# Performance work log

Measured on AMD Instinct MI355X. Metric: run time of the kernel, lower is better.

## Reference

```python
import jax, jax.numpy as jnp
import numpy as np

N_NODES = 50000
N_EDGES = 800000
NODE_DIM = 8
EDGE_DIM = 4
ENC = 64
ROUNDS = 3
OUT_DIM = 5
NEG_SLOPE = 0.2


def _segment_softmax(s, dst, n):
    # per-destination-neighborhood softmax over edge scores s: [E]
    smax = jax.ops.segment_max(s, dst, num_segments=n)
    ex = jnp.exp(s - smax[dst])
    denom = jax.ops.segment_sum(ex, dst, num_segments=n)
    return ex / denom[dst]


def _gatv2(h, e_enc, src, dst, Wl, Wr, We, att, b):
    # GATv2Conv, heads=1, share_weights=False, no dropout (eval)
    xl = h @ Wl            # [N, ENC] source transform
    xr = h @ Wr            # [N, ENC] dest transform
    ep = e_enc @ We        # [E, ENC] edge transform
    m = xl[src] + xr[dst] + ep               # [E, ENC]
    s = jax.nn.leaky_relu(m, NEG_SLOPE) @ att  # [E]
    alpha = _segment_softmax(s, dst, h.shape[0])
    out = jax.ops.segment_sum(alpha[:, None] * xl[src], dst, num_segments=h.shape[0])
    return out + b


def _gnn_stack(h, e_enc, src, dst, Wl, Wr, We, att, b):
    for r in range(ROUNDS):
        h = _gatv2(h, e_enc, src, dst, Wl[r], Wr[r], We[r], att[r], b[r])
        if r < ROUNDS - 1:
            h = jax.nn.relu(h)
    return h


def setup_inputs() -> dict:
    key = jax.random.key(0)
    ks = jax.random.split(key, 24)
    f32 = jnp.float32
    p = lambda k, shp: 0.1 * jax.random.normal(k, shp, dtype=f32)
    return {
        "x": jax.random.normal(ks[0], (N_NODES, NODE_DIM), dtype=f32),
        "edge_attr": jax.random.normal(ks[1], (N_EDGES, EDGE_DIM), dtype=f32),
        "W_node": p(ks[2], (NODE_DIM, ENC)), "b_node": jnp.zeros((ENC,), f32),
        "W_edge": p(ks[3], (EDGE_DIM, ENC)), "b_edge": jnp.zeros((ENC,), f32),
        "actor_Wl": p(ks[4], (ROUNDS, ENC, ENC)),
        "actor_Wr": p(ks[5], (ROUNDS, ENC, ENC)),
        "actor_We": p(ks[6], (ROUNDS, ENC, ENC)),
        "actor_att": p(ks[7], (ROUNDS, ENC)),
        "actor_b": jnp.zeros((ROUNDS, ENC), f32),
        "critic_Wl": p(ks[8], (ROUNDS, ENC, ENC)),
        "critic_Wr": p(ks[9], (ROUNDS, ENC, ENC)),
        "critic_We": p(ks[10], (ROUNDS, ENC, ENC)),
        "critic_att": p(ks[11], (ROUNDS, ENC)),
        "critic_b": jnp.zeros((ROUNDS, ENC), f32),
        "W_act": p(ks[12], (ENC, OUT_DIM)), "b_act": jnp.zeros((OUT_DIM,), f32),
        "W_val": p(ks[13], (ENC, 1)), "b_val": jnp.zeros((1,), f32),
        "src": jax.random.randint(ks[14], (N_EDGES,), 0, N_NODES, dtype=jnp.int32),
        "dst": jax.random.randint(ks[15], (N_EDGES,), 0, N_NODES, dtype=jnp.int32),
    }


def reference(x, edge_attr, W_node, b_node, W_edge, b_edge,
              actor_Wl, actor_Wr, actor_We, actor_att, actor_b,
              critic_Wl, critic_Wr, critic_We, critic_att, critic_b,
              W_act, b_act, W_val, b_val, src, dst):
    h0 = x @ W_node + b_node          # node encoder (single SlimFC, no activation)
    e0 = edge_attr @ W_edge + b_edge  # edge encoder
    ha = _gnn_stack(h0, e0, src, dst, actor_Wl, actor_Wr, actor_We, actor_att, actor_b)
    hc = _gnn_stack(h0, e0, src, dst, critic_Wl, critic_Wr, critic_We, critic_att, critic_b)
    actions = jnp.tanh(ha @ W_act + b_act)  # action decoder, tanh activation
    values = hc @ W_val + b_val             # value decoder, no activation
    return jnp.concatenate([actions, values], axis=-1)  # [N, OUT_DIM+1]
```

## Files before the change

kernel.cpp:

```cpp
#include <hip/hip_runtime.h>
#include <math.h>

#define N_NODES 50000
#define N_EDGES 800000
#define ENC 64
#define ROUNDS 3
#define NEG_SLOPE 0.2f

typedef unsigned int u32;

__device__ __forceinline__ float lrelu(float m) {
  return m > 0.f ? m : NEG_SLOPE * m;
}

__global__ void k_hist(const int* __restrict__ dst, int* __restrict__ deg) {
  int i = blockIdx.x * blockDim.x + threadIdx.x;
  int stride = gridDim.x * blockDim.x;
  for (; i < N_EDGES; i += stride) atomicAdd(&deg[dst[i]], 1);
}

#define SCAN_BLOCKS ((N_NODES + 255) / 256)

__global__ void __launch_bounds__(256) k_red(const int* __restrict__ deg,
                                             int* __restrict__ part) {
  __shared__ int sm[256];
  int bi = blockIdx.x, t = threadIdx.x;
  int i = bi * 256 + t;
  sm[t] = (i < N_NODES) ? deg[i] : 0;
  __syncthreads();
  for (int off = 128; off > 0; off >>= 1) {
    if (t < off) sm[t] += sm[t + off];
    __syncthreads();
  }
  if (t == 0) part[bi] = sm[0];
}

__global__ void __launch_bounds__(256) k_scanp(int* __restrict__ part) {
  __shared__ int sm[256];
  int t = threadIdx.x;
  int v = (t < SCAN_BLOCKS) ? part[t] : 0;
  sm[t] = v;
  __syncthreads();
  for (int off = 1; off < 256; off <<= 1) {
    int u = (t >= off) ? sm[t - off] : 0;
    __syncthreads();
    sm[t] += u;
    __syncthreads();
  }
  if (t < SCAN_BLOCKS) part[t] = sm[t] - v;
}

__global__ void __launch_bounds__(256) k_csr(int* __restrict__ degcur,
                                             const int* __restrict__ part,
                                             int* __restrict__ row_start) {
  __shared__ int sm[256];
  int bi = blockIdx.x, t = threadIdx.x;
  int i = bi * 256 + t;
  int v = (i < N_NODES) ? degcur[i] : 0;
  sm[t] = v;
  __syncthreads();
  for (int off = 1; off < 256; off <<= 1) {
    int u = (t >= off) ? sm[t - off] : 0;
    __syncthreads();
    sm[t] += u;
    __syncthreads();
  }
  int excl = sm[t] - v + part[bi];
  if (i < N_NODES) {
    row_start[i] = excl;
    degcur[i] = excl;
    if (i == N_NODES - 1) row_start[N_NODES] = excl + v;
  }
}

__global__ void k_scatter(const int* __restrict__ src, const int* __restrict__ dst,
                          const float* __restrict__ ea, int* __restrict__ cursor,
                          int* __restrict__ srcs, float* __restrict__ ea_perm) {
  int i = blockIdx.x * blockDim.x + threadIdx.x;
  int stride = gridDim.x * blockDim.x;
  for (; i < N_EDGES; i += stride) {
    int d = dst[i];
    int pos = atomicAdd(&cursor[d], 1);
    srcs[pos] = src[i];
    ((float4*)ea_perm)[pos] = ((const float4*)ea)[i];
  }
}

__global__ void k_wcomb(const float* __restrict__ W_edge, const float* __restrict__ b_edge,
                        const float* __restrict__ aWe, const float* __restrict__ cWe,
                        float* __restrict__ wcomb, float* __restrict__ bcomb) {
  int t = threadIdx.x;
  int i = t >> 6, d = t & 63;
  for (int sr = 0; sr < 6; ++sr) {
    const float* We = (sr < 3) ? (aWe + sr * ENC * ENC) : (cWe + (sr - 3) * ENC * ENC);
    float sum = 0.f;
    for (int k = 0; k < ENC; ++k) sum += W_edge[i * ENC + k] * We[k * ENC + d];
    wcomb[sr * 4 * ENC + i * ENC + d] = sum;
    if (t < ENC) {
      float bs = 0.f;
      for (int k = 0; k < ENC; ++k) bs += b_edge[k] * We[k * ENC + t];
      bcomb[sr * ENC + t] = bs;
    }
  }
}

__global__ void k_encode(const float* __restrict__ x, const float* __restrict__ Wn,
                         const float* __restrict__ bn, float* __restrict__ h0) {
  __shared__ float lw[8 * ENC];
  __shared__ float lb[ENC];
  int t = threadIdx.x;
  for (int i = t; i < 8 * ENC; i += blockDim.x) lw[i] = Wn[i];
  if (t < ENC) lb[t] = bn[t];
  __syncthreads();
  int wid = t >> 6, lane = t & 63;
  int nwaves = (blockDim.x >> 6) * gridDim.x;
  int w = blockIdx.x * (blockDim.x >> 6) + wid;
  for (int n = w; n < N_NODES; n += nwaves) {
    const float4* xr4 = (const float4*)(x + n * 8);
    float4 a = xr4[0], b = xr4[1];
    float acc = lb[lane];
    acc += a.x * lw[0 * ENC + lane] + a.y * lw[1 * ENC + lane] +
           a.z * lw[2 * ENC + lane] + a.w * lw[3 * ENC + lane];
    acc += b.x * lw[4 * ENC + lane] + b.y * lw[5 * ENC + lane] +
           b.z * lw[6 * ENC + lane] + b.w * lw[7 * ENC + lane];
    h0[n * ENC + lane] = acc;
  }
}

__global__ void __launch_bounds__(256) k_gemm2(const float* __restrict__ hinA,
                                               const float* __restrict__ hinC,
                                               const float* __restrict__ WlA,
                                               const float* __restrict__ WrA,
                                               const float* __restrict__ bcA,
                                               float* __restrict__ xlA_,
                                               float* __restrict__ xrA_,
                                               const float* __restrict__ WlC,
                                               const float* __restrict__ WrC,
                                               const float* __restrict__ bcC,
                                               float* __restrict__ xlC_,
                                               float* __restrict__ xrC_) {
  const int stk = blockIdx.y;
  const float* hin = stk ? hinC : hinA;
  const float* Wl = stk ? WlC : WlA;
  const float* Wr = stk ? WrC : WrA;
  const float* bc = stk ? bcC : bcA;
  float* xl = stk ? xlC_ : xlA_;
  float* xr = stk ? xrC_ : xrA_;
  __shared__ float lw[2 * ENC * ENC];
  __shared__ float lh[64 * ENC];
  int t = threadIdx.x;
  {
    const float4* wl4 = (const float4*)Wl;
    const float4* wr4 = (const float4*)Wr;
    float4* lw4 = (float4*)lw;
#pragma unroll
    for (int i = 0; i < 4; ++i) lw4[t + 256 * i] = wl4[t + 256 * i];
#pragma unroll
    for (int i = 0; i < 4; ++i) lw4[1024 + t + 256 * i] = wr4[t + 256 * i];
  }
  int base = blockIdx.x * 64;
  {
    const float4* h4 = (const float4*)hin;
    float4* lh4 = (float4*)lh;
    int maxi = N_NODES * 16 - 1;
#pragma unroll
    for (int i = 0; i < 4; ++i) {
      int idx = t + 256 * i;
      int gi = base * 16 + idx;
      if (gi > maxi) gi = maxi;
      lh4[idx] = h4[gi];
    }
  }
  __syncthreads();
  int wid = t >> 6, lane = t & 63;
  int msel = lane >> 5, cc = lane & 31;
  const float2* lw2 = (const float2*)lw;
  float* outp = msel ? xr : xl;
  float2 bcv = make_float2(0.f, 0.f);
  if (msel) bcv = ((const float2*)bc)[cc];
#pragma unroll
  for (int chunk = 0; chunk < 4; ++chunk) {
    int n0 = wid * 16 + chunk * 4;
    float a00 = 0.f, a01 = 0.f, a10 = 0.f, a11 = 0.f;
    float a20 = 0.f, a21 = 0.f, a30 = 0.f, a31 = 0.f;
    const float4* r0 = (const float4*)(lh + (n0 + 0) * ENC);
    const float4* r1 = (const float4*)(lh + (n0 + 1) * ENC);
    const float4* r2 = (const float4*)(lh + (n0 + 2) * ENC);
    const float4* r3 = (const float4*)(lh + (n0 + 3) * ENC);
#pragma unroll
    for (int k4 = 0; k4 < 16; ++k4) {
      float4 h0 = r0[k4], h1 = r1[k4], h2 = r2[k4], h3 = r3[k4];
      float2 w0 = lw2[msel * 2048 + (k4 * 4 + 0) * 32 + cc];
      float2 w1 = lw2[msel * 2048 + (k4 * 4 + 1) * 32 + cc];
      float2 w2 = lw2[msel * 2048 + (k4 * 4 + 2) * 32 + cc];
      float2 w3 = lw2[msel * 2048 + (k4 * 4 + 3) * 32 + cc];
      a00 += h0.x * w0.x + h0.y * w1.x + h0.z * w2.x + h0.w * w3.x;
      a01 += h0.x * w0.y + h0.y * w1.y + h0.z * w2.y + h0.w * w3.y;
      a10 += h1.x * w0.x + h1.y * w1.x + h1.z * w2.x + h1.w * w3.x;
      a11 += h1.x * w0.y + h1.y * w1.y + h1.z * w2.y + h1.w * w3.y;
      a20 += h2.x * w0.x + h2.y * w1.x + h2.z * w2.x + h2.w * w3.x;
      a21 += h2.x * w0.y + h2.y * w1.y + h2.z * w2.y + h2.w * w3.y;
      a30 += h3.x * w0.x + h3.y * w1.x + h3.z * w2.x + h3.w * w3.x;
      a31 += h3.x * w0.y + h3.y * w1.y + h3.z * w2.y + h3.w * w3.y;
    }
    int ng = base + n0;
    if (ng + 0 < N_NODES) *(float2*)(outp + (size_t)(ng + 0) * ENC + cc * 2) = make_float2(a00 + bcv.x, a01 + bcv.y);
    if (ng + 1 < N_NODES) *(float2*)(outp + (size_t)(ng + 1) * ENC + cc * 2) = make_float2(a10 + bcv.x, a11 + bcv.y);
    if (ng + 2 < N_NODES) *(float2*)(outp + (size_t)(ng + 2) * ENC + cc * 2) = make_float2(a20 + bcv.x, a21 + bcv.y);
    if (ng + 3 < N_NODES) *(float2*)(outp + (size_t)(ng + 3) * ENC + cc * 2) = make_float2(a30 + bcv.x, a31 + bcv.y);
  }
}

template <int RELU>
__global__ void __launch_bounds__(256) k_attn(
    const int* __restrict__ row_start, const int* __restrict__ srcs,
    const float* __restrict__ ea_perm,
    const float* __restrict__ xla, const float* __restrict__ xra,
    const float* __restrict__ xlc, const float* __restrict__ xrc,
    const float* __restrict__ wca, const float* __restrict__ wcc,
    const float* __restrict__ atta, const float* __restrict__ attc,
    const float* __restrict__ Ba, const float* __restrict__ Bc,
    float* __restrict__ ha, float* __restrict__ hc) {
  const float NEG_INF = __int_as_float(0xff800000u);
  int t = threadIdx.x;
  int wid = t >> 6, lane = t & 63;
  int g = lane >> 4;
  int l16 = lane & 15;
  float4 wa0 = ((const float4*)(wca + 0 * ENC))[l16];
  float4 wa1 = ((const float4*)(wca + 1 * ENC))[l16];
  float4 wa2 = ((const float4*)(wca + 2 * ENC))[l16];
  float4 wa3 = ((const float4*)(wca + 3 * ENC))[l16];
  float4 wc0 = ((const float4*)(wcc + 0 * ENC))[l16];
  float4 wc1 = ((const float4*)(wcc + 1 * ENC))[l16];
  float4 wc2 = ((const float4*)(wcc + 2 * ENC))[l16];
  float4 wc3 = ((const float4*)(wcc + 3 * ENC))[l16];
  float4 ata = ((const float4*)atta)[l16];
  float4 atc = ((const float4*)attc)[l16];
  float4 bva = ((const float4*)Ba)[l16];
  float4 bvc = ((const float4*)Bc)[l16];
  int nw = (blockDim.x >> 6) * gridDim.x;
  for (int n = blockIdx.x * (blockDim.x >> 6) + wid; n < N_NODES; n += nw) {
    int rs = row_start[n], re = row_start[n + 1];
    float4 outa, outc;
    if (re > rs) {
      float4 xran = ((const float4*)(xra + (size_t)n * ENC))[l16];
      float4 xrcn = ((const float4*)(xrc + (size_t)n * ENC))[l16];
      float ma = -1e30f, mc = -1e30f, dena = 0.f, denc = 0.f;
      float4 acca = make_float4(0.f, 0.f, 0.f, 0.f);
      float4 accc = make_float4(0.f, 0.f, 0.f, 0.f);
      for (int base = rs; base < re; base += 16) {
        int cnt = re - base;
        if (cnt > 16) cnt = 16;
        float eav = (lane < 4 * cnt) ? ea_perm[(size_t)base * 4 + lane] : 0.f;
        int sval = (lane < cnt) ? srcs[base + lane] : 0;
#pragma unroll
        for (int j = 0; j < 4; ++j) {
          if (j * 4 >= cnt) break;
          int jj = j * 4 + g;
          bool act = jj < cnt;
          int sn = __shfl(sval, act ? jj : 0);
          float av0 = __shfl(eav, jj * 4 + 0);
          float av1 = __shfl(eav, jj * 4 + 1);
          float av2 = __shfl(eav, jj * 4 + 2);
          float av3 = __shfl(eav, jj * 4 + 3);
          int idx = sn * 16 + l16;
          float4 la = ((const float4*)xla)[idx];
          float4 lc = ((const float4*)xlc)[idx];
          float px = lrelu(la.x + xran.x + av0 * wa0.x + av1 * wa1.x + av2 * wa2.x + av3 * wa3.x) * ata.x;
          px += lrelu(la.y + xran.y + av0 * wa0.y + av1 * wa1.y + av2 * wa2.y + av3 * wa3.y) * ata.y;
          px += lrelu(la.z + xran.z + av0 * wa0.z + av1 * wa1.z + av2 * wa2.z + av3 * wa3.z) * ata.z;
          px += lrelu(la.w + xran.w + av0 * wa0.w + av1 * wa1.w + av2 * wa2.w + av3 * wa3.w) * ata.w;
          float py = lrelu(lc.x + xrcn.x + av0 * wc0.x + av1 * wc1.x + av2 * wc2.x + av3 * wc3.x) * atc.x;
          py += lrelu(lc.y + xrcn.y + av0 * wc0.y + av1 * wc1.y + av2 * wc2.y + av3 * wc3.y) * atc.y;
          py += lrelu(lc.z + xrcn.z + av0 * wc0.z + av1 * wc1.z + av2 * wc2.z + av3 * wc3.z) * atc.z;
          py += lrelu(lc.w + xrcn.w + av0 * wc0.w + av1 * wc1.w + av2 * wc2.w + av3 * wc3.w) * atc.w;
          px += __shfl_xor(px, 1); py += __shfl_xor(py, 1);
          px += __shfl_xor(px, 2); py += __shfl_xor(py, 2);
          px += __shfl_xor(px, 4); py += __shfl_xor(py, 4);
          px += __shfl_xor(px, 8); py += __shfl_xor(py, 8);
          px = act ? px : NEG_INF;
          py = act ? py : NEG_INF;
          float mna = fmaxf(ma, px);
          float sca = __expf(ma - mna);
          float exa = __expf(px - mna);
          dena = dena * sca + exa;
          acca.x = acca.x * sca + exa * la.x;
          acca.y = acca.y * sca + exa * la.y;
          acca.z = acca.z * sca + exa * la.z;
          acca.w = acca.w * sca + exa * la.w;
          ma = mna;
          float mnc = fmaxf(mc, py);
          float scc = __expf(mc - mnc);
          float exc = __expf(py - mnc);
          denc = denc * scc + exc;
          accc.x = accc.x * scc + exc * lc.x;
          accc.y = accc.y * scc + exc * lc.y;
          accc.z = accc.z * scc + exc * lc.z;
          accc.w = accc.w * scc + exc * lc.w;
          mc = mnc;
        }
      }
#pragma unroll
      for (int d = 16; d <= 32; d <<= 1) {
        float m2 = __shfl_xor(ma, d);
        float dn2 = __shfl_xor(dena, d);
        float a2x = __shfl_xor(acca.x, d), a2y = __shfl_xor(acca.y, d);
        float a2z = __shfl_xor(acca.z, d), a2w = __shfl_xor(acca.w, d);
        float mn = fmaxf(ma, m2);
        float s1 = __expf(ma - mn), s2 = __expf(m2 - mn);
        dena = dena * s1 + dn2 * s2;
        acca.x = acca.x * s1 + a2x * s2;
        acca.y = acca.y * s1 + a2y * s2;
        acca.z = acca.z * s1 + a2z * s2;
        acca.w = acca.w * s1 + a2w * s2;
        ma = mn;
        m2 = __shfl_xor(mc, d);
        dn2 = __shfl_xor(denc, d);
        a2x = __shfl_xor(accc.x, d); a2y = __shfl_xor(accc.y, d);
        a2z = __shfl_xor(accc.z, d); a2w = __shfl_xor(accc.w, d);
        mn = fmaxf(mc, m2);
        s1 = __expf(mc - mn); s2 = __expf(m2 - mn);
        denc = denc * s1 + dn2 * s2;
        accc.x = accc.x * s1 + a2x * s2;
        accc.y = accc.y * s1 + a2y * s2;
        accc.z = accc.z * s1 + a2z * s2;
        accc.w = accc.w * s1 + a2w * s2;
        mc = mn;
      }
      float ia = 1.f / dena, ic = 1.f / denc;
      outa = make_float4(acca.x * ia + bva.x, acca.y * ia + bva.y,
                         acca.z * ia + bva.z, acca.w * ia + bva.w);
      outc = make_float4(accc.x * ic + bvc.x, accc.y * ic + bvc.y,
                         accc.z * ic + bvc.z, accc.w * ic + bvc.w);
    } else {
      outa = bva;
      outc = bvc;
    }
    if (RELU) {
      outa.x = fmaxf(outa.x, 0.f); outa.y = fmaxf(outa.y, 0.f);
      outa.z = fmaxf(outa.z, 0.f); outa.w = fmaxf(outa.w, 0.f);
      outc.x = fmaxf(outc.x, 0.f); outc.y = fmaxf(outc.y, 0.f);
      outc.z = fmaxf(outc.z, 0.f); outc.w = fmaxf(outc.w, 0.f);
    }
    if (g == 0) {
      ((float4*)(ha + (size_t)n * ENC))[l16] = outa;
      ((float4*)(hc + (size_t)n * ENC))[l16] = outc;
    }
  }
}

__global__ void k_dec(const float* __restrict__ ha, const float* __restrict__ hc,
                      const float* __restrict__ Wa, const float* __restrict__ ba,
                      const float* __restrict__ Wv, const float* __restrict__ bv,
                      float* __restrict__ out) {
  int t = threadIdx.x;
  int wid = t >> 6, lane = t & 63;
  int nw = (blockDim.x >> 6) * gridDim.x;
  int w = blockIdx.x * (blockDim.x >> 6) + wid;
  for (int n = w; n < N_NODES; n += nw) {
    float hva = ha[(size_t)n * ENC + lane];
    float hvc = hc[(size_t)n * ENC + lane];
#pragma unroll
    for (int j = 0; j < 5; ++j) {
      float p = hva * Wa[lane * 5 + j];
      p += __shfl_xor(p, 1);
      p += __shfl_xor(p, 2);
      p += __shfl_xor(p, 4);
      p += __shfl_xor(p, 8);
      p += __shfl_xor(p, 16);
      p += __shfl_xor(p, 32);
      if (lane == 0) out[n * 6 + j] = tanhf(p + ba[j]);
    }
    float p = hvc * Wv[lane];
    p += __shfl_xor(p, 1);
    p += __shfl_xor(p, 2);
    p += __shfl_xor(p, 4);
    p += __shfl_xor(p, 8);
    p += __shfl_xor(p, 16);
    p += __shfl_xor(p, 32);
    if (lane == 0) out[n * 6 + 5] = p + bv[0];
  }
}

extern "C" void kernel_launch(void* const* d_in, const int* in_sizes, int n_in,
                              void* d_out, int out_size, void* d_ws, size_t ws_size,
                              hipStream_t stream) {
  const float* x    = (const float*)d_in[0];
  const float* ea   = (const float*)d_in[1];
  const float* Wn   = (const float*)d_in[2];
  const float* bn   = (const float*)d_in[3];
  const float* Wedg = (const float*)d_in[4];
  const float* bedg = (const float*)d_in[5];
  const float* aWl  = (const float*)d_in[6];
  const float* aWr  = (const float*)d_in[7];
  const float* aWe  = (const float*)d_in[8];
  const float* aAtt = (const float*)d_in[9];
  const float* aB   = (const float*)d_in[10];
  const float* cWl  = (const float*)d_in[11];
  const float* cWr  = (const float*)d_in[12];
  const float* cWe  = (const float*)d_in[13];
  const float* cAtt = (const float*)d_in[14];
  const float* cB   = (const float*)d_in[15];
  const float* Wa   = (const float*)d_in[16];
  const float* ba   = (const float*)d_in[17];
  const float* Wv   = (const float*)d_in[18];
  const float* bv   = (const float*)d_in[19];
  const int* src    = (const int*)d_in[20];
  const int* dst    = (const int*)d_in[21];
  float* out = (float*)d_out;

  char* w = (char*)d_ws;
  size_t off = 0;
  auto alloc = [&](size_t bytes) -> char* {
    char* p = w + off;
    off = (off + bytes + 255) & ~(size_t)255;
    return p;
  };
  float* h0  = (float*)alloc((size_t)N_NODES * ENC * 4);
  float* hA  = (float*)alloc((size_t)N_NODES * ENC * 4);
  float* hC  = (float*)alloc((size_t)N_NODES * ENC * 4);
  float* xlA = (float*)alloc((size_t)N_NODES * ENC * 4);
  float* xrA = (float*)alloc((size_t)N_NODES * ENC * 4);
  float* xlC = (float*)alloc((size_t)N_NODES * ENC * 4);
  float* xrC = (float*)alloc((size_t)N_NODES * ENC * 4);
  int* srcs      = (int*)alloc((size_t)N_EDGES * 4);
  float* ea_perm = (float*)alloc((size_t)N_EDGES * 16);
  int* row_start = (int*)alloc((size_t)(N_NODES + 1) * 4);
  int* cursor    = (int*)alloc((size_t)N_NODES * 4);
  int* part      = (int*)alloc(256 * 4);
  float* wcomb   = (float*)alloc(6 * 4 * ENC * 4);
  float* bcomb   = (float*)alloc(6 * ENC * 4);

  hipMemsetAsync(cursor, 0, (size_t)N_NODES * 4, stream);
  k_hist<<<2048, 256, 0, stream>>>(dst, cursor);
  k_red<<<SCAN_BLOCKS, 256, 0, stream>>>(cursor, part);
  k_scanp<<<1, 256, 0, stream>>>(part);
  k_csr<<<SCAN_BLOCKS, 256, 0, stream>>>(cursor, part, row_start);
  k_scatter<<<2048, 256, 0, stream>>>(src, dst, ea, cursor, srcs, ea_perm);

  k_wcomb<<<1, 256, 0, stream>>>(Wedg, bedg, aWe, cWe, wcomb, bcomb);
  k_encode<<<512, 256, 0, stream>>>(x, Wn, bn, h0);

  const int GEMM_TILES = (N_NODES + 63) / 64;

  for (int r = 0; r < ROUNDS; ++r) {
    const float* hinA = (r == 0) ? h0 : hA;
    const float* hinC = (r == 0) ? h0 : hC;
    k_gemm2<<<dim3(GEMM_TILES, 2), 256, 0, stream>>>(
        hinA, hinC, aWl + r * ENC * ENC, aWr + r * ENC * ENC, bcomb + r * ENC, xlA, xrA,
        cWl + r * ENC * ENC, cWr + r * ENC * ENC, bcomb + (3 + r) * ENC, xlC, xrC);
    if (r < ROUNDS - 1)
      k_attn<1><<<2048, 256, 0, stream>>>(row_start, srcs, ea_perm, xlA, xrA, xlC, xrC,
                                          wcomb + r * 4 * ENC, wcomb + (3 + r) * 4 * ENC,
                                          aAtt + r * ENC, cAtt + r * ENC,
                                          aB + r * ENC, cB + r * ENC, hA, hC);
    else
      k_attn<0><<<2048, 256, 0, stream>>>(row_start, srcs, ea_perm, xlA, xrA, xlC, xrC,
                                          wcomb + r * 4 * ENC, wcomb + (3 + r) * 4 * ENC,
                                          aAtt + r * ENC, cAtt + r * ENC,
                                          aB + r * ENC, cB + r * ENC, hA, hC);
  }
  k_dec<<<1024, 256, 0, stream>>>(hA, hC, Wa, ba, Wv, bv, out);
}
```

Baseline: 787.6 us.

## Split attention kernel by actor/critic stack and prefetch next edge chunk

The attention kernel now handles one stack per block via blockIdx.y instead of processing actor and critic together in each wave. This halves register pressure per wave and doubles the grid. Within each chunk, all four neighbour gathers are issued before any compute, and the next chunk's source indices and edge attributes are prefetched, to overlap memory latency. The weight-combination kernel is folded into block 0 of the encode kernel to save a launch. The trade-off is that CSR metadata and edge attributes are now read twice, once per stack.

```diff
diff --git a/kernel.cpp b/kernel.cpp
--- a/kernel.cpp
+++ b/kernel.cpp
@@ -86,29 +86,28 @@
   }
 }
 
-__global__ void k_wcomb(const float* __restrict__ W_edge, const float* __restrict__ b_edge,
-                        const float* __restrict__ aWe, const float* __restrict__ cWe,
-                        float* __restrict__ wcomb, float* __restrict__ bcomb) {
-  int t = threadIdx.x;
-  int i = t >> 6, d = t & 63;
-  for (int sr = 0; sr < 6; ++sr) {
-    const float* We = (sr < 3) ? (aWe + sr * ENC * ENC) : (cWe + (sr - 3) * ENC * ENC);
-    float sum = 0.f;
-    for (int k = 0; k < ENC; ++k) sum += W_edge[i * ENC + k] * We[k * ENC + d];
-    wcomb[sr * 4 * ENC + i * ENC + d] = sum;
-    if (t < ENC) {
-      float bs = 0.f;
-      for (int k = 0; k < ENC; ++k) bs += b_edge[k] * We[k * ENC + t];
-      bcomb[sr * ENC + t] = bs;
-    }
-  }
-}
-
 __global__ void k_encode(const float* __restrict__ x, const float* __restrict__ Wn,
-                         const float* __restrict__ bn, float* __restrict__ h0) {
+                         const float* __restrict__ bn, float* __restrict__ h0,
+                         const float* __restrict__ W_edge, const float* __restrict__ b_edge,
+                         const float* __restrict__ aWe, const float* __restrict__ cWe,
+                         float* __restrict__ wcomb, float* __restrict__ bcomb) {
   __shared__ float lw[8 * ENC];
   __shared__ float lb[ENC];
   int t = threadIdx.x;
+  if (blockIdx.x == 0) {
+    int i = t >> 6, d = t & 63;
+    for (int sr = 0; sr < 6; ++sr) {
+      const float* We = (sr < 3) ? (aWe + sr * ENC * ENC) : (cWe + (sr - 3) * ENC * ENC);
+      float sum = 0.f;
+      for (int k = 0; k < ENC; ++k) sum += W_edge[i * ENC + k] * We[k * ENC + d];
+      wcomb[sr * 4 * ENC + i * ENC + d] = sum;
+      if (t < ENC) {
+        float bs = 0.f;
+        for (int k = 0; k < ENC; ++k) bs += b_edge[k] * We[k * ENC + t];
+        bcomb[sr * ENC + t] = bs;
+      }
+    }
+  }
   for (int i = t; i < 8 * ENC; i += blockDim.x) lw[i] = Wn[i];
   if (t < ENC) lb[t] = bn[t];
   __syncthreads();
@@ -222,130 +221,112 @@
     const float* __restrict__ Ba, const float* __restrict__ Bc,
     float* __restrict__ ha, float* __restrict__ hc) {
   const float NEG_INF = __int_as_float(0xff800000u);
+  const int stk = blockIdx.y;
+  const float* xl = stk ? xlc : xla;
+  const float* xr = stk ? xrc : xra;
+  const float* wc = stk ? wcc : wca;
+  const float* att = stk ? attc : atta;
+  const float* B = stk ? Bc : Ba;
+  float* hout = stk ? hc : ha;
   int t = threadIdx.x;
   int wid = t >> 6, lane = t & 63;
   int g = lane >> 4;
   int l16 = lane & 15;
-  float4 wa0 = ((const float4*)(wca + 0 * ENC))[l16];
-  float4 wa1 = ((const float4*)(wca + 1 * ENC))[l16];
-  float4 wa2 = ((const float4*)(wca + 2 * ENC))[l16];
-  float4 wa3 = ((const float4*)(wca + 3 * ENC))[l16];
-  float4 wc0 = ((const float4*)(wcc + 0 * ENC))[l16];
-  float4 wc1 = ((const float4*)(wcc + 1 * ENC))[l16];
-  float4 wc2 = ((const float4*)(wcc + 2 * ENC))[l16];
-  float4 wc3 = ((const float4*)(wcc + 3 * ENC))[l16];
-  float4 ata = ((const float4*)atta)[l16];
-  float4 atc = ((const float4*)attc)[l16];
-  float4 bva = ((const float4*)Ba)[l16];
-  float4 bvc = ((const float4*)Bc)[l16];
+  float4 w0 = ((const float4*)(wc + 0 * ENC))[l16];
+  float4 w1 = ((const float4*)(wc + 1 * ENC))[l16];
+  float4 w2 = ((const float4*)(wc + 2 * ENC))[l16];
+  float4 w3 = ((const float4*)(wc + 3 * ENC))[l16];
+  float4 at = ((const float4*)att)[l16];
+  float4 bv = ((const float4*)B)[l16];
   int nw = (blockDim.x >> 6) * gridDim.x;
   for (int n = blockIdx.x * (blockDim.x >> 6) + wid; n < N_NODES; n += nw) {
     int rs = row_start[n], re = row_start[n + 1];
-    float4 outa, outc;
+    float4 outv;
     if (re > rs) {
-      float4 xran = ((const float4*)(xra + (size_t)n * ENC))[l16];
-      float4 xrcn = ((const float4*)(xrc + (size_t)n * ENC))[l16];
-      float ma = -1e30f, mc = -1e30f, dena = 0.f, denc = 0.f;
-      float4 acca = make_float4(0.f, 0.f, 0.f, 0.f);
-      float4 accc = make_float4(0.f, 0.f, 0.f, 0.f);
+      float4 xrn = ((const float4*)(xr + (size_t)n * ENC))[l16];
+      float m = -1e30f, den = 0.f;
+      float4 acc = make_float4(0.f, 0.f, 0.f, 0.f);
+      int cnt0 = re - rs; if (cnt0 > 16) cnt0 = 16;
+      float eav = (lane < 4 * cnt0) ? ea_perm[(size_t)rs * 4 + lane] : 0.f;
+      int sval = (lane < cnt0) ? srcs[rs + lane] : 0;
       for (int base = rs; base < re; base += 16) {
-        int cnt = re - base;
-        if (cnt > 16) cnt = 16;
-        float eav = (lane < 4 * cnt) ? ea_perm[(size_t)base * 4 + lane] : 0.f;
-        int sval = (lane < cnt) ? srcs[base + lane] : 0;
+        int cnt = re - base; if (cnt > 16) cnt = 16;
+        float eav_c = eav;
+        int sval_c = sval;
+        int nb = base + 16;
+        if (nb < re) {
+          int cn = re - nb; if (cn > 16) cn = 16;
+          eav = (lane < 4 * cn) ? ea_perm[(size_t)nb * 4 + lane] : 0.f;
+          sval = (lane < cn) ? srcs[nb + lane] : 0;
+        }
+        float4 la[4];
+        bool act[4];
 #pragma unroll
         for (int j = 0; j < 4; ++j) {
-          if (j * 4 >= cnt) break;
           int jj = j * 4 + g;
-          bool act = jj < cnt;
-          int sn = __shfl(sval, act ? jj : 0);
-          float av0 = __shfl(eav, jj * 4 + 0);
-          float av1 = __shfl(eav, jj * 4 + 1);
-          float av2 = __shfl(eav, jj * 4 + 2);
-          float av3 = __shfl(eav, jj * 4 + 3);
-          int idx = sn * 16 + l16;
-          float4 la = ((const float4*)xla)[idx];
-          float4 lc = ((const float4*)xlc)[idx];
-          float px = lrelu(la.x + xran.x + av0 * wa0.x + av1 * wa1.x + av2 * wa2.x + av3 * wa3.x) * ata.x;
-          px += lrelu(la.y + xran.y + av0 * wa0.y + av1 * wa1.y + av2 * wa2.y + av3 * wa3.y) * ata.y;
-          px += lrelu(la.z + xran.z + av0 * wa0.z + av1 * wa1.z + av2 * wa2.z + av3 * wa3.z) * ata.z;
-          px += lrelu(la.w + xran.w + av0 * wa0.w + av1 * wa1.w + av2 * wa2.w + av3 * wa3.w) * ata.w;
-          float py = lrelu(lc.x + xrcn.x + av0 * wc0.x + av1 * wc1.x + av2 * wc2.x + av3 * wc3.x) * atc.x;
-          py += lrelu(lc.y + xrcn.y + av0 * wc0.y + av1 * wc1.y + av2 * wc2.y + av3 * wc3.y) * atc.y;
-          py += lrelu(lc.z + xrcn.z + av0 * wc0.z + av1 * wc1.z + av2 * wc2.z + av3 * wc3.z) * atc.z;
-          py += lrelu(lc.w + xrcn.w + av0 * wc0.w + av1 * wc1.w + av2 * wc2.w + av3 * wc3.w) * atc.w;
-          px += __shfl_xor(px, 1); py += __shfl_xor(py, 1);
-          px += __shfl_xor(px, 2); py += __shfl_xor(py, 2);
-          px += __shfl_xor(px, 4); py += __shfl_xor(py, 4);
-          px += __shfl_xor(px, 8); py += __shfl_xor(py, 8);
-          px = act ? px : NEG_INF;
-          py = act ? py : NEG_INF;
-          float mna = fmaxf(ma, px);
-          float sca = __expf(ma - mna);
-          float exa = __expf(px - mna);
-          dena = dena * sca + exa;
-          acca.x = acca.x * sca + exa * la.x;
-          acca.y = acca.y * sca + exa * la.y;
-          acca.z = acca.z * sca + exa * la.z;
-          acca.w = acca.w * sca + exa * la.w;
-          ma = mna;
-          float mnc = fmaxf(mc, py);
-          float scc = __expf(mc - mnc);
-          float exc = __expf(py - mnc);
-          denc = denc * scc + exc;
-          accc.x = accc.x * scc + exc * lc.x;
-          accc.y = accc.y * scc + exc * lc.y;
-          accc.z = accc.z * scc + exc * lc.z;
-          accc.w = accc.w * scc + exc * lc.w;
-          mc = mnc;
+          act[j] = jj < cnt;
+          int sj = __shfl(sval_c, act[j] ? jj : (cnt - 1));
+          la[j] = ((const float4*)xl)[sj * 16 + l16];
+        }
+        float px[4];
+#pragma unroll
+        for (int j = 0; j < 4; ++j) {
+          int jj = j * 4 + g;
+          float av0 = __shfl(eav_c, jj * 4 + 0);
+          float av1 = __shfl(eav_c, jj * 4 + 1);
+          float av2 = __shfl(eav_c, jj * 4 + 2);
+          float av3 = __shfl(eav_c, jj * 4 + 3);
+          float p = lrelu(la[j].x + xrn.x + av0 * w0.x + av1 * w1.x + av2 * w2.x + av3 * w3.x) * at.x;
+          p += lrelu(la[j].y + xrn.y + av0 * w0.y + av1 * w1.y + av2 * w2.y + av3 * w3.y) * at.y;
+          p += lrelu(la[j].z + xrn.z + av0 * w0.z + av1 * w1.z + av2 * w2.z + av3 * w3.z) * at.z;
+          p += lrelu(la[j].w + xrn.w + av0 * w0.w + av1 * w1.w + av2 * w2.w + av3 * w3.w) * at.w;
+          p += __shfl_xor(p, 1);
+          p += __shfl_xor(p, 2);
+          p += __shfl_xor(p, 4);
+          p += __shfl_xor(p, 8);
+          px[j] = act[j] ? p : NEG_INF;
+        }
+#pragma unroll
+        for (int j = 0; j < 4; ++j) {
+          float mn = fmaxf(m, px[j]);
+          float sc = __expf(m - mn);
+          float ex = __expf(px[j] - mn);
+          den = den * sc + ex;
+          acc.x = acc.x * sc + ex * la[j].x;
+          acc.y = acc.y * sc + ex * la[j].y;
+          acc.z = acc.z * sc + ex * la[j].z;
+          acc.w = acc.w * sc + ex * la[j].w;
+          m = mn;
         }
       }
 #pragma unroll
       for (int d = 16; d <= 32; d <<= 1) {
-        float m2 = __shfl_xor(ma, d);
-        float dn2 = __shfl_xor(dena, d);
-        float a2x = __shfl_xor(acca.x, d), a2y = __shfl_xor(acca.y, d);
-        float a2z = __shfl_xor(acca.z, d), a2w = __shfl_xor(acca.w, d);
-        float mn = fmaxf(ma, m2);
-        float s1 = __expf(ma - mn), s2 = __expf(m2 - mn);
-        dena = dena * s1 + dn2 * s2;
-        acca.x = acca.x * s1 + a2x * s2;
-        acca.y = acca.y * s1 + a2y * s2;
-        acca.z = acca.z * s1 + a2z * s2;
-        acca.w = acca.w * s1 + a2w * s2;
-        ma = mn;
-        m2 = __shfl_xor(mc, d);
-        dn2 = __shfl_xor(denc, d);
-        a2x = __shfl_xor(accc.x, d); a2y = __shfl_xor(accc.y, d);
-        a2z = __shfl_xor(accc.z, d); a2w = __shfl_xor(accc.w, d);
-        mn = fmaxf(mc, m2);
-        s1 = __expf(mc - mn); s2 = __expf(m2 - mn);
-        denc = denc * s1 + dn2 * s2;
-        accc.x = accc.x * s1 + a2x * s2;
-        accc.y = accc.y * s1 + a2y * s2;
-        accc.z = accc.z * s1 + a2z * s2;
-        accc.w = accc.w * s1 + a2w * s2;
-        mc = mn;
+        float m2 = __shfl_xor(m, d);
+        float dn2 = __shfl_xor(den, d);
+        float a2x = __shfl_xor(acc.x, d), a2y = __shfl_xor(acc.y, d);
+        float a2z = __shfl_xor(acc.z, d), a2w = __shfl_xor(acc.w, d);
+        float mn = fmaxf(m, m2);
+        float s1 = __expf(m - mn), s2 = __expf(m2 - mn);
+        den = den * s1 + dn2 * s2;
+        acc.x = acc.x * s1 + a2x * s2;
+        acc.y = acc.y * s1 + a2y * s2;
+        acc.z = acc.z * s1 + a2z * s2;
+        acc.w = acc.w * s1 + a2w * s2;
+        m = mn;
       }
-      float ia = 1.f / dena, ic = 1.f / denc;
-      outa = make_float4(acca.x * ia + bva.x, acca.y * ia + bva.y,
-                         acca.z * ia + bva.z, acca.w * ia + bva.w);
-      outc = make_float4(accc.x * ic + bvc.x, accc.y * ic + bvc.y,
-                         accc.z * ic + bvc.z, accc.w * ic + bvc.w);
+      float inv = 1.f / den;
+      outv = make_float4(acc.x * inv + bv.x, acc.y * inv + bv.y,
+                         acc.z * inv + bv.z, acc.w * inv + bv.w);
     } else {
-      outa = bva;
-      outc = bvc;
+      outv = bv;
     }
     if (RELU) {
-      outa.x = fmaxf(outa.x, 0.f); outa.y = fmaxf(outa.y, 0.f);
-      outa.z = fmaxf(outa.z, 0.f); outa.w = fmaxf(outa.w, 0.f);
-      outc.x = fmaxf(outc.x, 0.f); outc.y = fmaxf(outc.y, 0.f);
-      outc.z = fmaxf(outc.z, 0.f); outc.w = fmaxf(outc.w, 0.f);
-    }
-    if (g == 0) {
-      ((float4*)(ha + (size_t)n * ENC))[l16] = outa;
-      ((float4*)(hc + (size_t)n * ENC))[l16] = outc;
-    }
+      outv.x = fmaxf(outv.x, 0.f);
+      outv.y = fmaxf(outv.y, 0.f);
+      outv.z = fmaxf(outv.z, 0.f);
+      outv.w = fmaxf(outv.w, 0.f);
+    }
+    if (g == 0) ((float4*)(hout + (size_t)n * ENC))[l16] = outv;
   }
 }
 
@@ -438,8 +419,7 @@
   k_csr<<<SCAN_BLOCKS, 256, 0, stream>>>(cursor, part, row_start);
   k_scatter<<<2048, 256, 0, stream>>>(src, dst, ea, cursor, srcs, ea_perm);
 
-  k_wcomb<<<1, 256, 0, stream>>>(Wedg, bedg, aWe, cWe, wcomb, bcomb);
-  k_encode<<<512, 256, 0, stream>>>(x, Wn, bn, h0);
+  k_encode<<<512, 256, 0, stream>>>(x, Wn, bn, h0, Wedg, bedg, aWe, cWe, wcomb, bcomb);
 
   const int GEMM_TILES = (N_NODES + 63) / 64;
 
@@ -450,15 +430,15 @@
         hinA, hinC, aWl + r * ENC * ENC, aWr + r * ENC * ENC, bcomb + r * ENC, xlA, xrA,
         cWl + r * ENC * ENC, cWr + r * ENC * ENC, bcomb + (3 + r) * ENC, xlC, xrC);
     if (r < ROUNDS - 1)
-      k_attn<1><<<2048, 256, 0, stream>>>(row_start, srcs, ea_perm, xlA, xrA, xlC, xrC,
-                                          wcomb + r * 4 * ENC, wcomb + (3 + r) * 4 * ENC,
-                                          aAtt + r * ENC, cAtt + r * ENC,
-                                          aB + r * ENC, cB + r * ENC, hA, hC);
+      k_attn<1><<<dim3(2048, 2), 256, 0, stream>>>(row_start, srcs, ea_perm, xlA, xrA, xlC, xrC,
+                                                   wcomb + r * 4 * ENC, wcomb + (3 + r) * 4 * ENC,
+                                                   aAtt + r * ENC, cAtt + r * ENC,
+                                                   aB + r * ENC, cB + r * ENC, hA, hC);
     else
-      k_attn<0><<<2048, 256, 0, stream>>>(row_start, srcs, ea_perm, xlA, xrA, xlC, xrC,
-                                          wcomb + r * 4 * ENC, wcomb + (3 + r) * 4 * ENC,
-                                          aAtt + r * ENC, cAtt + r * ENC,
-                                          aB + r * ENC, cB + r * ENC, hA, hC);
+      k_attn<0><<<dim3(2048, 2), 256, 0, stream>>>(row_start, srcs, ea_perm, xlA, xrA, xlC, xrC,
+                                                   wcomb + r * 4 * ENC, wcomb + (3 + r) * 4 * ENC,
+                                                   aAtt + r * ENC, cAtt + r * ENC,
+                                                   aB + r * ENC, cB + r * ENC, hA, hC);
   }
   k_dec<<<1024, 256, 0, stream>>>(hA, hC, Wa, ba, Wv, bv, out);
 }
```

Result: slower. 845.6 us (+7.4%).
